# Kernel tuning notes

Measured on AMD Instinct MI355X. Metric: run time of the kernel, lower is better.

The kernel has to match this reference:

```python
import jax, jax.numpy as jnp
import numpy as np

H_DIM = 64
GRID = 8
NBR = 2.0
BN_EPS = 1e-5
N_SEQ = 64
N_PED = 64
BOTTLENECK = 1024


def setup_inputs() -> dict:
    key = jax.random.key(0)
    k0, k1, k2, k3 = jax.random.split(key, 4)
    batch = N_SEQ * N_PED
    h_states = jax.random.normal(k0, (1, batch, H_DIM), jnp.float32)
    # positions spread over a 4x4 area so some neighbors fall inside the 2.0 neighborhood
    end_pos = jax.random.uniform(k1, (batch, 2), jnp.float32) * 4.0
    rel_pos = jax.random.normal(k2, (batch, 2), jnp.float32)
    starts = jnp.arange(N_SEQ, dtype=jnp.int32) * N_PED
    seq_start_end = jnp.stack([starts, starts + N_PED], axis=1)
    in_dim = GRID * GRID * H_DIM  # 4096
    W = jax.random.normal(k3, (in_dim, BOTTLENECK), jnp.float32) / np.sqrt(in_dim)
    b = jnp.zeros((BOTTLENECK,), jnp.float32)
    gamma = jnp.ones((BOTTLENECK,), jnp.float32)
    beta = jnp.zeros((BOTTLENECK,), jnp.float32)
    return {"h_states": h_states, "seq_start_end": seq_start_end, "end_pos": end_pos,
            "rel_pos": rel_pos, "W": W, "b": b, "gamma": gamma, "beta": beta}


def _pool_scene(hidden, pos):
    # hidden: (n, h), pos: (n, 2). Pair (i, j): ped j binned into ped i's grid.
    n, h = hidden.shape
    g2 = GRID * GRID
    half = NBR / 2.0
    tl_x = pos[:, 0] - half
    tl_y = pos[:, 1] + half
    br_x = pos[:, 0] + half
    br_y = pos[:, 1] - half
    px = pos[None, :, 0]  # (1, n) -> broadcast over i
    py = pos[None, :, 1]
    cell_x = jnp.floor((px - tl_x[:, None]) / NBR * GRID)
    cell_y = jnp.floor((tl_y[:, None] - py) / NBR * GRID)
    grid = (cell_x + cell_y * GRID).astype(jnp.int32) + 1  # slot 0 = trash bin
    oob = ((px >= br_x[:, None]) | (px <= tl_x[:, None]) |
           (py >= tl_y[:, None]) | (py <= br_y[:, None]) |
           jnp.eye(n, dtype=bool))  # self-interaction excluded
    grid = grid + (jnp.arange(n, dtype=jnp.int32) * g2)[:, None]
    grid = jnp.where(oob, 0, grid)  # (n, n)
    src = jnp.broadcast_to(hidden[None], (n, n, h)).reshape(-1, h)
    buf = jnp.zeros((n * g2 + 1, h), hidden.dtype).at[grid.reshape(-1)].add(src)
    return buf[1:].reshape(n, g2 * h)


def reference(h_states, seq_start_end, end_pos, rel_pos, W, b, gamma, beta):
    batch = end_pos.shape[0]
    n_seq = seq_start_end.shape[0]
    n_ped = batch // n_seq  # equal-length scenes by construction
    hid = h_states.reshape(-1, H_DIM).reshape(n_seq, n_ped, H_DIM)
    pos = end_pos.reshape(n_seq, n_ped, 2)
    pool_h = jax.vmap(_pool_scene)(hid, pos).reshape(batch, -1)  # (batch, 4096)
    x = pool_h @ W + b
    # BatchNorm1d in training mode (batch statistics, biased variance)
    mean = jnp.mean(x, axis=0)
    var = jnp.var(x, axis=0)
    x = (x - mean) * jax.lax.rsqrt(var + BN_EPS) * gamma + beta
    return jax.nn.relu(x)
```

## Files before the change

kernel.cpp:

```cpp
#include <hip/hip_runtime.h>
#include <hip/hip_bf16.h>


#define NPED  64
#define BATCH 4096
#define HDIM  64
#define G2    64
#define KDIM  4096
#define NOUT  1024

typedef __attribute__((ext_vector_type(8))) short short8;
typedef __attribute__((ext_vector_type(4))) float f32x4;

__device__ __forceinline__ unsigned short f2bf(float f) {
    __hip_bfloat16 h = __float2bfloat16(f);
    return *reinterpret_cast<unsigned short*>(&h);
}

__device__ __forceinline__ void lds_load16(const void* g, void* l) {
    __builtin_amdgcn_global_load_lds(
        (const __attribute__((address_space(1))) void*)g,
        (__attribute__((address_space(3))) void*)l, 16, 0, 0);
}

__global__ __launch_bounds__(512) void pool_kernel(const float* __restrict__ h,
                                                   const float* __restrict__ pos,
                                                   unsigned short* __restrict__ A2) {
    __shared__ float hs[NPED * HDIM];
    __shared__ float pl[NPED * 2];
    int t = threadIdx.x;
    int w = t >> 6, lane = t & 63;
    int p0 = blockIdx.x * 8;
    int sbase = p0 & ~(NPED - 1);
    if (t < 128) pl[t] = pos[sbase * 2 + t];
    {
        const float4* src = (const float4*)(h + (size_t)sbase * HDIM);
        float4* dst = (float4*)hs;
        dst[t] = src[t];
        dst[t + 512] = src[t + 512];
    }
    __syncthreads();

    int i = p0 + w;
    int il = i & (NPED - 1);
    float cx0 = pl[2 * il], cy0 = pl[2 * il + 1];
    float tlx = cx0 - 1.f, tly = cy0 + 1.f, brx = cx0 + 1.f, bry = cy0 - 1.f;
    float px = pl[2 * lane], py = pl[2 * lane + 1];
    bool inb = (lane != il) && !(px >= brx || px <= tlx || py >= tly || py <= bry);
    int cellx = (int)floorf((px - tlx) * 4.f);
    int celly = (int)floorf((tly - py) * 4.f);
    int cell = cellx + celly * 8;
    inb = inb && ((unsigned)cell < 64u);

    int mtile = i >> 4, r = i & 15;
    unsigned short* outb = A2 + (size_t)mtile * 65536 + r * 8
                              + (lane >> 5) * 512 + ((lane >> 3) & 3) * 128 + (lane & 7);
    const float* hrow = hs + lane;
    #pragma unroll
    for (int c = 0; c < 64; ++c) {
        unsigned long long m = __ballot(inb && (cell == c));
        float a = 0.f;
        while (m) {
            int j = __builtin_ctzll(m);
            m &= m - 1;
            a += hrow[j * HDIM];
        }
        outb[c * 1024] = f2bf(a);
    }
}

__global__ __launch_bounds__(256) void wt_kernel(const float* __restrict__ W,
                                                 unsigned short* __restrict__ Wt,
                                                 float* __restrict__ stats) {
    __shared__ unsigned short tile[64][66];
    int k0 = blockIdx.x * 64;
    int n0 = blockIdx.y * 64;
    int t = threadIdx.x;
    if (blockIdx.x == 0 && blockIdx.y < 8) stats[blockIdx.y * 256 + t] = 0.f;
    #pragma unroll
    for (int p = 0; p < 4; ++p) {
        int lin = p * 256 + t;
        int c4 = lin & 15, kl = lin >> 4;
        float4 v = ((const float4*)(W + (size_t)(k0 + kl) * NOUT + n0))[c4];
        tile[c4 * 4 + 0][kl] = f2bf(v.x);
        tile[c4 * 4 + 1][kl] = f2bf(v.y);
        tile[c4 * 4 + 2][kl] = f2bf(v.z);
        tile[c4 * 4 + 3][kl] = f2bf(v.w);
    }
    __syncthreads();
    unsigned int* out = (unsigned int*)Wt;
    #pragma unroll
    for (int p = 0; p < 8; ++p) {
        int lin = p * 256 + t;
        int ku = lin & 31, nl = lin >> 5;
        unsigned int v = (unsigned int)tile[nl][2 * ku] |
                         ((unsigned int)tile[nl][2 * ku + 1] << 16);
        out[(size_t)(n0 + nl) * (KDIM / 2) + (k0 >> 1) + ku] = v;
    }
}

__global__ __launch_bounds__(256, 2) void gemm_kernel(const unsigned short* __restrict__ A2,
                                                      const unsigned short* __restrict__ Bt,
                                                      float* __restrict__ C,
                                                      float* __restrict__ P1,
                                                      float* __restrict__ P2,
                                                      float* __restrict__ P3) {
    __shared__ __align__(16) unsigned short Bs[128 * 64];
    int t = threadIdx.x;
    int w = t >> 6, lane = t & 63;
    int m0 = blockIdx.x * 256, n0 = blockIdx.y * 128;
    int kbase = blockIdx.z * 1024;
    int wm = w * 64;

    f32x4 acc[4][8];
    #pragma unroll
    for (int i = 0; i < 4; ++i)
        #pragma unroll
        for (int j = 0; j < 8; ++j)
            acc[i][j] = (f32x4){0.f, 0.f, 0.f, 0.f};

    int rbase = w * 32 + (lane >> 3);
    int koff = ((lane & 7) ^ (lane >> 3)) * 8;
    const unsigned short* Bg = Bt + (size_t)(n0 + rbase) * KDIM + kbase + koff;
    unsigned short* BsW = Bs + w * 2048 + lane * 8;

    const unsigned short* Abase = A2 + (size_t)((m0 + wm) >> 4) * 65536 + lane * 8;
    int ktile0 = kbase >> 5;

    for (int kt = 0; kt < 1024; kt += 64) {
        #pragma unroll
        for (int q = 0; q < 4; ++q)
            lds_load16(Bg + (size_t)q * 8 * KDIM + kt, BsW + q * 512);
        short8 af[2][4];
        int ktile = ktile0 + (kt >> 5);
        #pragma unroll
        for (int kk = 0; kk < 2; ++kk)
            #pragma unroll
            for (int i = 0; i < 4; ++i)
                af[kk][i] = *(const short8*)(Abase + ((size_t)i * 128 + ktile + kk) * 512);
        __syncthreads();
        #pragma unroll
        for (int kk = 0; kk < 2; ++kk) {
            int chunk = ((kk * 4 + (lane >> 4)) ^ (lane & 7)) * 8;
            #pragma unroll
            for (int j = 0; j < 8; ++j) {
                short8 b = *(const short8*)&Bs[(j * 16 + (lane & 15)) * 64 + chunk];
                #pragma unroll
                for (int i = 0; i < 4; ++i)
                    acc[i][j] = __builtin_amdgcn_mfma_f32_16x16x32_bf16(af[kk][i], b, acc[i][j], 0, 0, 0);
            }
        }
        __syncthreads();
    }

    float* dst = blockIdx.z == 0 ? C : blockIdx.z == 1 ? P1 : blockIdx.z == 2 ? P2 : P3;
    int col0 = n0 + (lane & 15);
    int row0 = m0 + wm + ((lane >> 4) << 2);
    #pragma unroll
    for (int i = 0; i < 4; ++i)
        #pragma unroll
        for (int j = 0; j < 8; ++j)
            #pragma unroll
            for (int r = 0; r < 4; ++r)
                dst[(size_t)(row0 + i * 16 + r) * NOUT + col0 + j * 16] = acc[i][j][r];
}

__global__ __launch_bounds__(256) void combine_stats(float* __restrict__ C,
                                                     const float* __restrict__ P1,
                                                     const float* __restrict__ P2,
                                                     const float* __restrict__ P3,
                                                     float* __restrict__ stats) {
    int t = threadIdx.x;
    int colchunk = blockIdx.x & 3;
    int rowchunk = blockIdx.x >> 2;
    int col = colchunk * 256 + t;
    size_t base = (size_t)rowchunk * 32 * NOUT + col;
    float s = 0.f, s2 = 0.f;
    #pragma unroll 4
    for (int r = 0; r < 32; ++r) {
        size_t ix = base + (size_t)r * NOUT;
        float v = (C[ix] + P1[ix]) + (P2[ix] + P3[ix]);
        C[ix] = v;
        s += v; s2 += v * v;
    }
    atomicAdd(&stats[col], s);
    atomicAdd(&stats[NOUT + col], s2);
}

__global__ __launch_bounds__(256) void norm_kernel(float* __restrict__ C,
                                                   const float* __restrict__ stats,
                                                   const float* __restrict__ gamma,
                                                   const float* __restrict__ beta) {
    int idx = blockIdx.x * 256 + threadIdx.x;
    int col4 = idx & 255;
    float4 x = ((const float4*)C)[idx];
    float4 s = ((const float4*)stats)[col4];
    float4 q = ((const float4*)(stats + NOUT))[col4];
    float4 g = ((const float4*)gamma)[col4];
    float4 b = ((const float4*)beta)[col4];
    const float inv_n = 1.f / 4096.f;
    float m, inv;
    m = s.x * inv_n; inv = rsqrtf(q.x * inv_n - m * m + 1e-5f); x.x = fmaxf((x.x - m) * inv * g.x + b.x, 0.f);
    m = s.y * inv_n; inv = rsqrtf(q.y * inv_n - m * m + 1e-5f); x.y = fmaxf((x.y - m) * inv * g.y + b.y, 0.f);
    m = s.z * inv_n; inv = rsqrtf(q.z * inv_n - m * m + 1e-5f); x.z = fmaxf((x.z - m) * inv * g.z + b.z, 0.f);
    m = s.w * inv_n; inv = rsqrtf(q.w * inv_n - m * m + 1e-5f); x.w = fmaxf((x.w - m) * inv * g.w + b.w, 0.f);
    ((float4*)C)[idx] = x;
}

extern "C" void kernel_launch(void* const* d_in, const int* in_sizes, int n_in,
                              void* d_out, int out_size, void* d_ws, size_t ws_size,
                              hipStream_t stream) {
    const float* h      = (const float*)d_in[0];
    const float* endpos = (const float*)d_in[2];
    const float* W      = (const float*)d_in[4];
    const float* gamma  = (const float*)d_in[6];
    const float* beta   = (const float*)d_in[7];
    float* C = (float*)d_out;

    char* ws = (char*)d_ws;
    size_t off = 0;
    unsigned short* A2 = (unsigned short*)(ws + off); off += (size_t)BATCH * KDIM * 2;
    unsigned short* Wt = (unsigned short*)(ws + off); off += (size_t)NOUT * KDIM * 2;
    float* P1 = (float*)(ws + off); off += (size_t)BATCH * NOUT * 4;
    float* P2 = (float*)(ws + off); off += (size_t)BATCH * NOUT * 4;
    float* P3 = (float*)(ws + off); off += (size_t)BATCH * NOUT * 4;
    float* stats = (float*)(ws + off);

    pool_kernel<<<BATCH / 8, 512, 0, stream>>>(h, endpos, A2);
    wt_kernel<<<dim3(KDIM / 64, NOUT / 64), 256, 0, stream>>>(W, Wt, stats);
    gemm_kernel<<<dim3(BATCH / 256, NOUT / 128, 4), 256, 0, stream>>>(A2, Wt, C, P1, P2, P3);
    combine_stats<<<512, 256, 0, stream>>>(C, P1, P2, P3, stats);
    norm_kernel<<<(BATCH * NOUT / 4) / 256, 256, 0, stream>>>(C, stats, gamma, beta);
}
```

Baseline: 150.9 us.

## Pre-tile W into MFMA fragment layout and load GEMM operands directly to registers

The weight transpose kernel now writes W in the same 16x32 MFMA fragment-tiled layout already used for the pooled activations. This lets the GEMM drop LDS staging and barriers and load both operands straight into registers, double-buffered across k-steps. The split-K factor drops from 4 to 2, which removes two fp32 partial buffers and their reads in the combine kernel. The trade-off is no cross-wave operand sharing through LDS, so each wave fetches its own B fragments from global or L2, and the grid is smaller (512 blocks of 128 threads).

Result: slower. 160.2 us (+6.2%).

```diff
diff --git a/kernel.cpp b/kernel.cpp
--- a/kernel.cpp
+++ b/kernel.cpp
@@ -15,12 +15,6 @@
 __device__ __forceinline__ unsigned short f2bf(float f) {
     __hip_bfloat16 h = __float2bfloat16(f);
     return *reinterpret_cast<unsigned short*>(&h);
-}
-
-__device__ __forceinline__ void lds_load16(const void* g, void* l) {
-    __builtin_amdgcn_global_load_lds(
-        (const __attribute__((address_space(1))) void*)g,
-        (__attribute__((address_space(3))) void*)l, 16, 0, 0);
 }
 
 __global__ __launch_bounds__(512) void pool_kernel(const float* __restrict__ h,
@@ -70,7 +64,7 @@
 }
 
 __global__ __launch_bounds__(256) void wt_kernel(const float* __restrict__ W,
-                                                 unsigned short* __restrict__ Wt,
+                                                 unsigned short* __restrict__ Wt2,
                                                  float* __restrict__ stats) {
     __shared__ unsigned short tile[64][66];
     int k0 = blockIdx.x * 64;
@@ -88,78 +82,78 @@
         tile[c4 * 4 + 3][kl] = f2bf(v.w);
     }
     __syncthreads();
-    unsigned int* out = (unsigned int*)Wt;
+    unsigned int* out = (unsigned int*)Wt2;
     #pragma unroll
     for (int p = 0; p < 8; ++p) {
         int lin = p * 256 + t;
-        int ku = lin & 31, nl = lin >> 5;
-        unsigned int v = (unsigned int)tile[nl][2 * ku] |
-                         ((unsigned int)tile[nl][2 * ku + 1] << 16);
-        out[(size_t)(n0 + nl) * (KDIM / 2) + (k0 >> 1) + ku] = v;
-    }
-}
-
-__global__ __launch_bounds__(256, 2) void gemm_kernel(const unsigned short* __restrict__ A2,
-                                                      const unsigned short* __restrict__ Bt,
-                                                      float* __restrict__ C,
-                                                      float* __restrict__ P1,
-                                                      float* __restrict__ P2,
-                                                      float* __restrict__ P3) {
-    __shared__ __align__(16) unsigned short Bs[128 * 64];
+        int qq = lin & 3;
+        int r = (lin >> 2) & 15;
+        int chunk = (lin >> 6) & 3;
+        int ktl = (lin >> 8) & 1;
+        int ntl = lin >> 9;
+        int nl = ntl * 16 + r;
+        int kl = ktl * 32 + chunk * 8 + qq * 2;
+        unsigned int v = (unsigned int)tile[nl][kl] |
+                         ((unsigned int)tile[nl][kl + 1] << 16);
+        out[(size_t)(blockIdx.y * 4 + ntl) * 32768 + (size_t)(blockIdx.x * 2 + ktl) * 256
+            + chunk * 64 + r * 4 + qq] = v;
+    }
+}
+
+__global__ __launch_bounds__(128) void gemm_kernel(const unsigned short* __restrict__ A2,
+                                                   const unsigned short* __restrict__ Wt2,
+                                                   float* __restrict__ C,
+                                                   float* __restrict__ P1) {
     int t = threadIdx.x;
     int w = t >> 6, lane = t & 63;
-    int m0 = blockIdx.x * 256, n0 = blockIdx.y * 128;
-    int kbase = blockIdx.z * 1024;
-    int wm = w * 64;
-
-    f32x4 acc[4][8];
-    #pragma unroll
-    for (int i = 0; i < 4; ++i)
-        #pragma unroll
-        for (int j = 0; j < 8; ++j)
+    int mtile0 = blockIdx.x * 16 + w * 8;
+    int ntile0 = blockIdx.y * 4;
+    int ktile0 = blockIdx.z * 64;
+
+    f32x4 acc[8][4];
+    #pragma unroll
+    for (int i = 0; i < 8; ++i)
+        #pragma unroll
+        for (int j = 0; j < 4; ++j)
             acc[i][j] = (f32x4){0.f, 0.f, 0.f, 0.f};
 
-    int rbase = w * 32 + (lane >> 3);
-    int koff = ((lane & 7) ^ (lane >> 3)) * 8;
-    const unsigned short* Bg = Bt + (size_t)(n0 + rbase) * KDIM + kbase + koff;
-    unsigned short* BsW = Bs + w * 2048 + lane * 8;
-
-    const unsigned short* Abase = A2 + (size_t)((m0 + wm) >> 4) * 65536 + lane * 8;
-    int ktile0 = kbase >> 5;
-
-    for (int kt = 0; kt < 1024; kt += 64) {
-        #pragma unroll
-        for (int q = 0; q < 4; ++q)
-            lds_load16(Bg + (size_t)q * 8 * KDIM + kt, BsW + q * 512);
-        short8 af[2][4];
-        int ktile = ktile0 + (kt >> 5);
-        #pragma unroll
-        for (int kk = 0; kk < 2; ++kk)
-            #pragma unroll
-            for (int i = 0; i < 4; ++i)
-                af[kk][i] = *(const short8*)(Abase + ((size_t)i * 128 + ktile + kk) * 512);
-        __syncthreads();
-        #pragma unroll
-        for (int kk = 0; kk < 2; ++kk) {
-            int chunk = ((kk * 4 + (lane >> 4)) ^ (lane & 7)) * 8;
-            #pragma unroll
-            for (int j = 0; j < 8; ++j) {
-                short8 b = *(const short8*)&Bs[(j * 16 + (lane & 15)) * 64 + chunk];
-                #pragma unroll
-                for (int i = 0; i < 4; ++i)
-                    acc[i][j] = __builtin_amdgcn_mfma_f32_16x16x32_bf16(af[kk][i], b, acc[i][j], 0, 0, 0);
-            }
+    const unsigned short* Ab = A2 + (size_t)mtile0 * 65536 + (size_t)ktile0 * 512 + lane * 8;
+    const unsigned short* Bb = Wt2 + (size_t)ntile0 * 65536 + (size_t)ktile0 * 512 + lane * 8;
+
+    short8 a_c[8], b_c[4], a_n[8], b_n[4];
+    #pragma unroll
+    for (int i = 0; i < 8; ++i) a_c[i] = *(const short8*)(Ab + (size_t)i * 65536);
+    #pragma unroll
+    for (int j = 0; j < 4; ++j) b_c[j] = *(const short8*)(Bb + (size_t)j * 65536);
+
+    #pragma unroll 2
+    for (int kt = 0; kt < 64; ++kt) {
+        if (kt < 63) {
+            const unsigned short* An = Ab + (size_t)(kt + 1) * 512;
+            const unsigned short* Bn = Bb + (size_t)(kt + 1) * 512;
+            #pragma unroll
+            for (int i = 0; i < 8; ++i) a_n[i] = *(const short8*)(An + (size_t)i * 65536);
+            #pragma unroll
+            for (int j = 0; j < 4; ++j) b_n[j] = *(const short8*)(Bn + (size_t)j * 65536);
         }
-        __syncthreads();
-    }
-
-    float* dst = blockIdx.z == 0 ? C : blockIdx.z == 1 ? P1 : blockIdx.z == 2 ? P2 : P3;
-    int col0 = n0 + (lane & 15);
-    int row0 = m0 + wm + ((lane >> 4) << 2);
-    #pragma unroll
-    for (int i = 0; i < 4; ++i)
-        #pragma unroll
-        for (int j = 0; j < 8; ++j)
+        #pragma unroll
+        for (int j = 0; j < 4; ++j)
+            #pragma unroll
+            for (int i = 0; i < 8; ++i)
+                acc[i][j] = __builtin_amdgcn_mfma_f32_16x16x32_bf16(a_c[i], b_c[j], acc[i][j], 0, 0, 0);
+        #pragma unroll
+        for (int i = 0; i < 8; ++i) a_c[i] = a_n[i];
+        #pragma unroll
+        for (int j = 0; j < 4; ++j) b_c[j] = b_n[j];
+    }
+
+    float* dst = blockIdx.z ? P1 : C;
+    int row0 = mtile0 * 16 + ((lane >> 4) << 2);
+    int col0 = ntile0 * 16 + (lane & 15);
+    #pragma unroll
+    for (int i = 0; i < 8; ++i)
+        #pragma unroll
+        for (int j = 0; j < 4; ++j)
             #pragma unroll
             for (int r = 0; r < 4; ++r)
                 dst[(size_t)(row0 + i * 16 + r) * NOUT + col0 + j * 16] = acc[i][j][r];
@@ -167,8 +161,6 @@
 
 __global__ __launch_bounds__(256) void combine_stats(float* __restrict__ C,
                                                      const float* __restrict__ P1,
-                                                     const float* __restrict__ P2,
-                                                     const float* __restrict__ P3,
                                                      float* __restrict__ stats) {
     int t = threadIdx.x;
     int colchunk = blockIdx.x & 3;
@@ -179,7 +171,7 @@
     #pragma unroll 4
     for (int r = 0; r < 32; ++r) {
         size_t ix = base + (size_t)r * NOUT;
-        float v = (C[ix] + P1[ix]) + (P2[ix] + P3[ix]);
+        float v = C[ix] + P1[ix];
         C[ix] = v;
         s += v; s2 += v * v;
     }
@@ -219,16 +211,14 @@
 
     char* ws = (char*)d_ws;
     size_t off = 0;
-    unsigned short* A2 = (unsigned short*)(ws + off); off += (size_t)BATCH * KDIM * 2;
-    unsigned short* Wt = (unsigned short*)(ws + off); off += (size_t)NOUT * KDIM * 2;
+    unsigned short* A2  = (unsigned short*)(ws + off); off += (size_t)BATCH * KDIM * 2;
+    unsigned short* Wt2 = (unsigned short*)(ws + off); off += (size_t)NOUT * KDIM * 2;
     float* P1 = (float*)(ws + off); off += (size_t)BATCH * NOUT * 4;
-    float* P2 = (float*)(ws + off); off += (size_t)BATCH * NOUT * 4;
-    float* P3 = (float*)(ws + off); off += (size_t)BATCH * NOUT * 4;
     float* stats = (float*)(ws + off);
 
     pool_kernel<<<BATCH / 8, 512, 0, stream>>>(h, endpos, A2);
-    wt_kernel<<<dim3(KDIM / 64, NOUT / 64), 256, 0, stream>>>(W, Wt, stats);
-    gemm_kernel<<<dim3(BATCH / 256, NOUT / 128, 4), 256, 0, stream>>>(A2, Wt, C, P1, P2, P3);
-    combine_stats<<<512, 256, 0, stream>>>(C, P1, P2, P3, stats);
+    wt_kernel<<<dim3(KDIM / 64, NOUT / 64), 256, 0, stream>>>(W, Wt2, stats);
+    gemm_kernel<<<dim3(16, 16, 2), 128, 0, stream>>>(A2, Wt2, C, P1);
+    combine_stats<<<512, 256, 0, stream>>>(C, P1, stats);
     norm_kernel<<<(BATCH * NOUT / 4) / 256, 256, 0, stream>>>(C, stats, gamma, beta);
 }
```

## Double-buffer B tiles in LDS and prefetch A fragments in GEMM

Applied to the files above, without the earlier changes.

Converts the GEMM main loop to a ping-pong scheme with two LDS buffers for B and two register sets for A fragments. The loads for the next K tile are issued before the MFMAs on the current tile, so global-to-LDS latency can hide behind compute, and one barrier per tile is removed. The cost is doubled LDS for B and extra VGPRs for the second A fragment set, which may pressure occupancy under the 2-blocks-per-SM launch bound.

New measurement: 154.9 us. 1.03x slower.

```diff
diff --git a/kernel.cpp b/kernel.cpp
--- a/kernel.cpp
+++ b/kernel.cpp
@@ -99,13 +99,29 @@
     }
 }
 
+__device__ __forceinline__ void do_phase(const unsigned short* __restrict__ Bcur,
+                                         const short8 af[2][4],
+                                         f32x4 acc[4][8], int lane) {
+    #pragma unroll
+    for (int kk = 0; kk < 2; ++kk) {
+        int chunk = ((kk * 4 + (lane >> 4)) ^ (lane & 7)) * 8;
+        #pragma unroll
+        for (int j = 0; j < 8; ++j) {
+            short8 b = *(const short8*)&Bcur[(j * 16 + (lane & 15)) * 64 + chunk];
+            #pragma unroll
+            for (int i = 0; i < 4; ++i)
+                acc[i][j] = __builtin_amdgcn_mfma_f32_16x16x32_bf16(af[kk][i], b, acc[i][j], 0, 0, 0);
+        }
+    }
+}
+
 __global__ __launch_bounds__(256, 2) void gemm_kernel(const unsigned short* __restrict__ A2,
                                                       const unsigned short* __restrict__ Bt,
                                                       float* __restrict__ C,
                                                       float* __restrict__ P1,
                                                       float* __restrict__ P2,
                                                       float* __restrict__ P3) {
-    __shared__ __align__(16) unsigned short Bs[128 * 64];
+    __shared__ __align__(16) unsigned short Bs[2][128 * 64];
     int t = threadIdx.x;
     int w = t >> 6, lane = t & 63;
     int m0 = blockIdx.x * 256, n0 = blockIdx.y * 128;
@@ -122,35 +138,49 @@
     int rbase = w * 32 + (lane >> 3);
     int koff = ((lane & 7) ^ (lane >> 3)) * 8;
     const unsigned short* Bg = Bt + (size_t)(n0 + rbase) * KDIM + kbase + koff;
-    unsigned short* BsW = Bs + w * 2048 + lane * 8;
+    int ldsoff = w * 2048 + lane * 8;
 
     const unsigned short* Abase = A2 + (size_t)((m0 + wm) >> 4) * 65536 + lane * 8;
-    int ktile0 = kbase >> 5;
-
-    for (int kt = 0; kt < 1024; kt += 64) {
+    int K50 = kbase >> 5;
+
+    #pragma unroll
+    for (int q = 0; q < 4; ++q)
+        lds_load16(Bg + (size_t)q * 8 * KDIM, &Bs[0][0] + ldsoff + q * 512);
+    short8 afA[2][4], afB[2][4];
+    #pragma unroll
+    for (int kk = 0; kk < 2; ++kk)
+        #pragma unroll
+        for (int i = 0; i < 4; ++i)
+            afA[kk][i] = *(const short8*)(Abase + ((size_t)i * 128 + K50 + kk) * 512);
+
+    for (int kt = 0; kt < 16; kt += 2) {
+        __syncthreads();
         #pragma unroll
         for (int q = 0; q < 4; ++q)
-            lds_load16(Bg + (size_t)q * 8 * KDIM + kt, BsW + q * 512);
-        short8 af[2][4];
-        int ktile = ktile0 + (kt >> 5);
-        #pragma unroll
-        for (int kk = 0; kk < 2; ++kk)
-            #pragma unroll
-            for (int i = 0; i < 4; ++i)
-                af[kk][i] = *(const short8*)(Abase + ((size_t)i * 128 + ktile + kk) * 512);
-        __syncthreads();
-        #pragma unroll
-        for (int kk = 0; kk < 2; ++kk) {
-            int chunk = ((kk * 4 + (lane >> 4)) ^ (lane & 7)) * 8;
-            #pragma unroll
-            for (int j = 0; j < 8; ++j) {
-                short8 b = *(const short8*)&Bs[(j * 16 + (lane & 15)) * 64 + chunk];
+            lds_load16(Bg + (size_t)q * 8 * KDIM + (kt + 1) * 64, &Bs[1][0] + ldsoff + q * 512);
+        {
+            int K5 = K50 + (kt + 1) * 2;
+            #pragma unroll
+            for (int kk = 0; kk < 2; ++kk)
                 #pragma unroll
                 for (int i = 0; i < 4; ++i)
-                    acc[i][j] = __builtin_amdgcn_mfma_f32_16x16x32_bf16(af[kk][i], b, acc[i][j], 0, 0, 0);
-            }
-        }
+                    afB[kk][i] = *(const short8*)(Abase + ((size_t)i * 128 + K5 + kk) * 512);
+        }
+        do_phase(&Bs[0][0], afA, acc, lane);
+
         __syncthreads();
+        if (kt + 2 < 16) {
+            #pragma unroll
+            for (int q = 0; q < 4; ++q)
+                lds_load16(Bg + (size_t)q * 8 * KDIM + (kt + 2) * 64, &Bs[0][0] + ldsoff + q * 512);
+            int K5 = K50 + (kt + 2) * 2;
+            #pragma unroll
+            for (int kk = 0; kk < 2; ++kk)
+                #pragma unroll
+                for (int i = 0; i < 4; ++i)
+                    afA[kk][i] = *(const short8*)(Abase + ((size_t)i * 128 + K5 + kk) * 512);
+        }
+        do_phase(&Bs[1][0], afB, acc, lane);
     }
 
     float* dst = blockIdx.z == 0 ? C : blockIdx.z == 1 ? P1 : blockIdx.z == 2 ? P2 : P3;
```
